# Kernel optimization log

Hardware: AMD Instinct MI355X
Metric: run time of the kernel (lower is better)

The kernel has to match this reference:

```python
import jax, jax.numpy as jnp
import numpy as np

B, N, C = 64, 197, 768
H, GH, D = 12, 2, 64           # num_heads, global_heads, head_dim
HR = H // GH                    # head_ratio = 6
TOTAL_HEADS = 2 * GH + H        # 16
SCALE = D ** -0.5
LEVELS = 3


def setup_inputs() -> dict:
    key = jax.random.key(0)
    ks = jax.random.split(key, 10)
    s = 0.02
    return {
        "x": jax.random.normal(ks[0], (B, N, C), jnp.float32),
        "qkv_w": jax.random.normal(ks[1], (C, TOTAL_HEADS * D), jnp.float32) * s,
        "qkv_b": jax.random.normal(ks[2], (TOTAL_HEADS * D,), jnp.float32) * s,
        "masks": jax.random.uniform(ks[3], (N, N, LEVELS), jnp.float32),
        "mask_proj": jnp.ones((LEVELS, H), jnp.float32),
        "mask_base": jax.random.normal(ks[4], (H,), jnp.float32) * s,
        "head_proj_w": jnp.eye(H, dtype=jnp.float32) + jax.random.normal(ks[5], (H, H), jnp.float32) * s,
        "head_proj_b": jax.random.normal(ks[6], (H,), jnp.float32) * s,
        "proj_w": jax.random.normal(ks[7], (C, C), jnp.float32) * s,
        "proj_b": jax.random.normal(ks[8], (C,), jnp.float32) * s,
    }


def reference(x, qkv_w, qkv_b, masks, mask_proj, mask_base, head_proj_w, head_proj_b, proj_w, proj_b):
    b, n, c = x.shape
    # fused qkv projection -> (b, total_heads, n, d)
    qkv = (x @ qkv_w + qkv_b).reshape(b, n, TOTAL_HEADS, D).transpose(0, 2, 1, 3)
    q = qkv[:, :GH]                 # (b, gh, n, d)
    k = qkv[:, GH:2 * GH]           # (b, gh, n, d)
    v = qkv[:, 2 * GH:]             # (b, h, n, d)

    # global-head attention scores (b, gh, n, n)
    attn = jnp.einsum("bgnd,bgmd->bgnm", q, k) * SCALE

    # per-pair learned mask weights: (n, n, levels) @ (levels, h) -> (n, n, h)
    mw = masks @ mask_proj + mask_base
    # reshape to (1, gh, n, n, hr) per global_proj_type='full'
    mw = mw.reshape(n, n, GH, HR).transpose(2, 0, 1, 3)[None]

    # modulate scores: (b, gh, n, n, hr)
    a = attn[..., None] * mw

    # non_linear head mixing: relu then per-position linear over heads
    a = a.transpose(0, 2, 3, 1, 4).reshape(b, n, n, H)   # (b, n, n, h)
    a = jax.nn.relu(a) @ head_proj_w + head_proj_b
    a = a.transpose(0, 3, 1, 2)                          # (b, h, n, n)

    a = jax.nn.softmax(a, axis=-1)
    out = jnp.einsum("bhnm,bhmd->bnhd", a, v).reshape(b, n, c)
    return out @ proj_w + proj_b
```

## Files before the change

### kernel.cpp

```cpp
#include <hip/hip_runtime.h>
#include <cstdint>
#include <cstddef>

#define BB   64
#define NN   197
#define CC   768
#define HH   12
#define THD  16
#define DD   64
#define MROWS (BB*NN)
#define QKVN (THD*DD)
#define SCALE_ 0.125f
#define ATTS 208
#define KPAD 224
#define SSTR 240

typedef unsigned short u16;
typedef __attribute__((ext_vector_type(2))) float f32x2;
typedef __attribute__((ext_vector_type(4))) float f32x4;
typedef __attribute__((ext_vector_type(8))) short s16x8;
typedef __attribute__((address_space(1))) unsigned int as1_u32;
typedef __attribute__((address_space(3))) unsigned int as3_u32;

__device__ __forceinline__ float bf2f(u16 u) {
  union { unsigned int i; float f; } x; x.i = ((unsigned int)u) << 16; return x.f;
}
__device__ __forceinline__ u16 f2bf(float f) {
  unsigned int x = __builtin_bit_cast(unsigned int, f);
  unsigned int r = (x + 0x7fffu + ((x >> 16) & 1u)) >> 16;
  return (u16)r;
}
__device__ __forceinline__ void gl_lds16(const u16* g, u16* l) {
  __builtin_amdgcn_global_load_lds((const as1_u32*)g, (as3_u32*)l, 16, 0, 0);
}

__global__ __launch_bounds__(256) void k_cvt_x(const float* __restrict__ src,
                                               u16* __restrict__ dst, int n8) {
  int i = blockIdx.x * 256 + threadIdx.x;
  if (i >= n8) return;
  const float4* s = (const float4*)src;
  float4 a = s[2 * i], b = s[2 * i + 1];
  ushort4 lo, hi;
  lo.x = f2bf(a.x); lo.y = f2bf(a.y); lo.z = f2bf(a.z); lo.w = f2bf(a.w);
  hi.x = f2bf(b.x); hi.y = f2bf(b.y); hi.z = f2bf(b.z); hi.w = f2bf(b.w);
  ((ushort4*)dst)[2 * i] = lo;
  ((ushort4*)dst)[2 * i + 1] = hi;
}

__global__ __launch_bounds__(256) void k_transpose(const float* __restrict__ in,
                                                   u16* __restrict__ out,
                                                   int R, int Ccol) {
  __shared__ u16 tile[32][33];
  int c0 = blockIdx.x * 32, r0 = blockIdx.y * 32;
  int tx = threadIdx.x & 31, ty = threadIdx.x >> 5;
#pragma unroll
  for (int i = 0; i < 32; i += 8) {
    int r = r0 + ty + i, c = c0 + tx;
    tile[ty + i][tx] = (r < R && c < Ccol) ? f2bf(in[(size_t)r * Ccol + c]) : (u16)0;
  }
  __syncthreads();
#pragma unroll
  for (int i = 0; i < 32; i += 8) {
    int cc = c0 + ty + i, rr = r0 + tx;
    if (cc < Ccol && rr < R) out[(size_t)cc * R + rr] = tile[tx][ty + i];
  }
}

__global__ __launch_bounds__(512, 2) void k_gemm_bt(const u16* __restrict__ A,
                                                    const u16* __restrict__ Bt,
                                                    const float* __restrict__ bias,
                                                    void* __restrict__ Cout,
                                                    int M, int Nn, int K,
                                                    int write_bf16) {
  __shared__ u16 As[2][2][256 * 32];
  __shared__ u16 Bs[2][2][256 * 32];
  int t = threadIdx.x;
  int w = t >> 6, lane = t & 63;

  int NT = gridDim.y;
  int nwg = gridDim.x * gridDim.y;
  int d = blockIdx.y * gridDim.x + blockIdx.x;
  int q8 = nwg >> 3, r8 = nwg & 7;
  int xcd = d & 7, j = d >> 3;
  int g = (xcd < r8 ? xcd * (q8 + 1) : r8 * (q8 + 1) + (xcd - r8) * q8) + j;
  int mt = g / NT, nt = g - mt * NT;
  int m0 = mt * 256, n0 = nt * 256;

  int wm = w >> 2, wn = w & 3;

  f32x4 acc[8][4];
#pragma unroll
  for (int i = 0; i < 8; i++)
#pragma unroll
    for (int j2 = 0; j2 < 4; j2++)
#pragma unroll
      for (int e = 0; e < 4; e++) acc[i][j2][e] = 0.f;

  int lrow4 = lane >> 2;
  int lkc = (lane & 3) * 8;

  auto stage = [&](int buf, int kbase) {
#pragma unroll
    for (int kh = 0; kh < 2; kh++) {
      int kk = kbase + kh * 32;
#pragma unroll
      for (int rc = 0; rc < 2; rc++) {
        int c = w + rc * 8;
        int row = c * 16 + lrow4;
        int ga = m0 + row; if (ga >= M) ga = M - 1;
        gl_lds16(A + (size_t)ga * K + kk + lkc, &As[buf][kh][c * 512]);
        gl_lds16(Bt + (size_t)(n0 + row) * K + kk + lkc, &Bs[buf][kh][c * 512]);
      }
    }
  };

  auto compute = [&](int buf) {
    int r16 = lane & 15, k8 = (lane >> 4) * 8;
#pragma unroll
    for (int kh = 0; kh < 2; kh++) {
      s16x8 af[8], bfv[4];
#pragma unroll
      for (int s = 0; s < 8; s++)
        af[s]  = *(const s16x8*)&As[buf][kh][(wm * 128 + s * 16 + r16) * 32 + k8];
#pragma unroll
      for (int s = 0; s < 4; s++)
        bfv[s] = *(const s16x8*)&Bs[buf][kh][(wn * 64 + s * 16 + r16) * 32 + k8];
#pragma unroll
      for (int sm = 0; sm < 8; sm++)
#pragma unroll
        for (int sn = 0; sn < 4; sn++)
          acc[sm][sn] = __builtin_amdgcn_mfma_f32_16x16x32_bf16(af[sm], bfv[sn], acc[sm][sn], 0, 0, 0);
    }
  };

  stage(0, 0);
  __syncthreads();
  int cur = 0;
  for (int k0 = 0; k0 < K; k0 += 64) {
    if (k0 + 64 < K) stage(cur ^ 1, k0 + 64);
    compute(cur);
    __syncthreads();
    cur ^= 1;
  }

  u16*   Cb = (u16*)Cout;
  float* Cf = (float*)Cout;
  int quad = lane >> 4, col = lane & 15;
#pragma unroll
  for (int sn = 0; sn < 4; sn++) {
    int gn = n0 + wn * 64 + sn * 16 + col;
    float bv = bias[gn];
#pragma unroll
    for (int sm = 0; sm < 8; sm++) {
      int gmb = m0 + wm * 128 + sm * 16 + quad * 4;
#pragma unroll
      for (int i = 0; i < 4; i++) {
        int gm = gmb + i;
        if (gm < M) {
          float v = acc[sm][sn][i] + bv;
          if (write_bf16) Cb[(size_t)gm * Nn + gn] = f2bf(v);
          else            Cf[(size_t)gm * Nn + gn] = v;
        }
      }
    }
  }
}

__global__ __launch_bounds__(256) void k_qk(const u16* __restrict__ qkv,
                                            float* __restrict__ att) {
  __shared__ u16 As[2][128 * 32];
  __shared__ u16 Bs[2][128 * 32];
  int t = threadIdx.x;
  int w = t >> 6, lane = t & 63;
  int bz = blockIdx.z, b = bz >> 1, g = bz & 1;
  int n0 = blockIdx.x * 128;
  int m0 = blockIdx.y * 128;
  int wm = w >> 1, wn = w & 1;

  f32x4 acc[4][4];
#pragma unroll
  for (int i = 0; i < 4; i++)
#pragma unroll
    for (int j = 0; j < 4; j++)
#pragma unroll
      for (int e = 0; e < 4; e++) acc[i][j][e] = 0.f;

  int lrow4 = lane >> 2, lkc = (lane & 3) * 8;

#pragma unroll
  for (int half = 0; half < 2; half++) {
    int kk = half * 32;
#pragma unroll
    for (int rc = 0; rc < 2; rc++) {
      int c = w + rc * 4;
      int row = c * 16 + lrow4;
      int nq = n0 + row; if (nq > NN - 1) nq = NN - 1;
      int mk = m0 + row; if (mk > NN - 1) mk = NN - 1;
      gl_lds16(qkv + (size_t)(b * NN + nq) * QKVN + g * DD + kk + lkc, &As[half][c * 512]);
      gl_lds16(qkv + (size_t)(b * NN + mk) * QKVN + 2 * DD + g * DD + kk + lkc, &Bs[half][c * 512]);
    }
  }
  __syncthreads();
  {
    int r16 = lane & 15, k8 = (lane >> 4) * 8;
#pragma unroll
    for (int half = 0; half < 2; half++) {
      s16x8 af[4], bfv[4];
#pragma unroll
      for (int s = 0; s < 4; s++) {
        af[s]  = *(const s16x8*)&As[half][(wm * 64 + s * 16 + r16) * 32 + k8];
        bfv[s] = *(const s16x8*)&Bs[half][(wn * 64 + s * 16 + r16) * 32 + k8];
      }
#pragma unroll
      for (int sm = 0; sm < 4; sm++)
#pragma unroll
        for (int sn = 0; sn < 4; sn++)
          acc[sm][sn] = __builtin_amdgcn_mfma_f32_16x16x32_bf16(af[sm], bfv[sn], acc[sm][sn], 0, 0, 0);
    }
  }
  int quad = lane >> 4, col = lane & 15;
#pragma unroll
  for (int sn = 0; sn < 4; sn++) {
    int gn = m0 + wn * 64 + sn * 16 + col;
#pragma unroll
    for (int sm = 0; sm < 4; sm++) {
      int gmb = n0 + wm * 64 + sm * 16 + quad * 4;
#pragma unroll
      for (int i = 0; i < 4; i++) {
        int gm = gmb + i;
        if (gm < NN && gn < NN)
          att[((size_t)bz * NN + gm) * ATTS + gn] = acc[sm][sn][i] * SCALE_;
      }
    }
  }
}

__global__ __launch_bounds__(256) void k_softmax_p(const float* __restrict__ att,
                                                   const float* __restrict__ masks,
                                                   const float* __restrict__ mproj,
                                                   const float* __restrict__ mbase,
                                                   const float* __restrict__ hpw,
                                                   const float* __restrict__ hpb,
                                                   u16* __restrict__ P) {
  __shared__ float S[12][SSTR];
  __shared__ f32x2 hpw_s[72];
  __shared__ f32x2 mp_s[18];
  __shared__ f32x2 mb_s[6], hpb_s[6];
  __shared__ float inv_s[12];
  int t = threadIdx.x;
  int n = blockIdx.x, b = blockIdx.y;

  if (t < 72) hpw_s[t] = ((const f32x2*)hpw)[t];
  if (t < 18) mp_s[t] = ((const f32x2*)mproj)[t];
  if (t < 6) { mb_s[t] = ((const f32x2*)mbase)[t]; hpb_s[t] = ((const f32x2*)hpb)[t]; }
  __syncthreads();

  if (t < NN) {
    int m = t;
    float a0 = att[((size_t)(b * 2 + 0) * NN + n) * ATTS + m];
    float a1 = att[((size_t)(b * 2 + 1) * NN + n) * ATTS + m];
    const float* mk = masks + ((size_t)n * NN + m) * 3;
    float l0 = mk[0], l1 = mk[1], l2 = mk[2];
    f32x2 pre2[6];
#pragma unroll
    for (int k = 0; k < 6; k++) {
      f32x2 wv = mb_s[k] + l0 * mp_s[k] + l1 * mp_s[6 + k] + l2 * mp_s[12 + k];
      float av = (k < 3) ? a0 : a1;
      f32x2 v = wv * av;
      pre2[k].x = v.x > 0.f ? v.x : 0.f;
      pre2[k].y = v.y > 0.f ? v.y : 0.f;
    }
    f32x2 s2[6];
#pragma unroll
    for (int k = 0; k < 6; k++) s2[k] = hpb_s[k];
#pragma unroll
    for (int h = 0; h < 12; h++) {
      float p = (h & 1) ? pre2[h >> 1].y : pre2[h >> 1].x;
#pragma unroll
      for (int k = 0; k < 6; k++) s2[k] += p * hpw_s[h * 6 + k];
    }
#pragma unroll
    for (int k = 0; k < 6; k++) {
      S[2 * k][m] = s2[k].x;
      S[2 * k + 1][m] = s2[k].y;
    }
  } else if (t < KPAD) {
#pragma unroll
    for (int h = 0; h < 12; h++) S[h][t] = 0.f;
  }
  __syncthreads();

  {
    int g = t >> 4, l16 = t & 15;
    if (g < 12) {
      float vals[13];
      float mx = -1e30f;
#pragma unroll
      for (int i = 0; i < 13; i++) {
        int m = l16 + i * 16;
        float x = S[g][m];
        vals[i] = (m < NN) ? x : -1e30f;
        mx = fmaxf(mx, vals[i]);
      }
#pragma unroll
      for (int off = 8; off; off >>= 1) mx = fmaxf(mx, __shfl_xor(mx, off, 16));
      float sum = 0.f;
#pragma unroll
      for (int i = 0; i < 13; i++) {
        int m = l16 + i * 16;
        float e = __expf(vals[i] - mx);
        if (m < NN) { S[g][m] = e; sum += e; }
      }
#pragma unroll
      for (int off = 8; off; off >>= 1) sum += __shfl_xor(sum, off, 16);
      if (l16 == 0) inv_s[g] = 1.f / sum;
    }
  }
  __syncthreads();

  for (int c4 = t; c4 < 672; c4 += 256) {
    int h = c4 / 56;
    int m = (c4 - h * 56) * 4;
    f32x4 v = *(const f32x4*)&S[h][m];
    float iv = inv_s[h];
    ushort4 u;
    u.x = f2bf(v.x * iv); u.y = f2bf(v.y * iv);
    u.z = f2bf(v.z * iv); u.w = f2bf(v.w * iv);
    *(ushort4*)(P + ((size_t)(b * HH + h) * NN + n) * KPAD + m) = u;
  }
}

__global__ __launch_bounds__(256) void k_pv(const u16* __restrict__ P,
                                            const u16* __restrict__ qkv,
                                            u16* __restrict__ aout) {
  __shared__ u16 As[2][128 * 32];
  __shared__ u16 Bs[2][64 * 32];
  int t = threadIdx.x;
  int w = t >> 6, lane = t & 63;
  int bh = blockIdx.y, b = bh / HH, h = bh - b * HH;
  int n0 = blockIdx.x * 128;

  f32x4 acc[2][4];
#pragma unroll
  for (int i = 0; i < 2; i++)
#pragma unroll
    for (int j = 0; j < 4; j++)
#pragma unroll
      for (int e = 0; e < 4; e++) acc[i][j][e] = 0.f;

  int lrow4 = lane >> 2, lkc = (lane & 3) * 8;
  int vml = t & 31, vd0 = (t >> 5) * 8;

  for (int k0 = 0; k0 < KPAD; k0 += 64) {
    int nh = (KPAD - k0 >= 64) ? 2 : 1;
    for (int half = 0; half < nh; half++) {
      int kk = k0 + half * 32;
#pragma unroll
      for (int rc = 0; rc < 2; rc++) {
        int c = w + rc * 4;
        int row = c * 16 + lrow4;
        int gn = n0 + row; if (gn > NN - 1) gn = NN - 1;
        gl_lds16(P + ((size_t)bh * NN + gn) * KPAD + kk + lkc, &As[half][c * 512]);
      }
      {
        int m = kk + vml;
        u16 v8[8];
        if (m < NN) {
          const ushort4* vp = (const ushort4*)(qkv + (size_t)(b * NN + m) * QKVN + (4 + h) * DD + vd0);
          ushort4 lo = vp[0], hi = vp[1];
          v8[0] = lo.x; v8[1] = lo.y; v8[2] = lo.z; v8[3] = lo.w;
          v8[4] = hi.x; v8[5] = hi.y; v8[6] = hi.z; v8[7] = hi.w;
        } else {
#pragma unroll
          for (int j = 0; j < 8; j++) v8[j] = 0;
        }
#pragma unroll
        for (int j = 0; j < 8; j++) Bs[half][(vd0 + j) * 32 + vml] = v8[j];
      }
    }
    __syncthreads();
    int r16 = lane & 15, k8 = (lane >> 4) * 8;
    for (int half = 0; half < nh; half++) {
      s16x8 af[2], bfv[4];
#pragma unroll
      for (int s = 0; s < 2; s++)
        af[s] = *(const s16x8*)&As[half][(w * 32 + s * 16 + r16) * 32 + k8];
#pragma unroll
      for (int s = 0; s < 4; s++)
        bfv[s] = *(const s16x8*)&Bs[half][(s * 16 + r16) * 32 + k8];
#pragma unroll
      for (int sm = 0; sm < 2; sm++)
#pragma unroll
        for (int sn = 0; sn < 4; sn++)
          acc[sm][sn] = __builtin_amdgcn_mfma_f32_16x16x32_bf16(af[sm], bfv[sn], acc[sm][sn], 0, 0, 0);
    }
    __syncthreads();
  }
  int quad = lane >> 4, col = lane & 15;
#pragma unroll
  for (int sn = 0; sn < 4; sn++) {
    int gd = sn * 16 + col;
#pragma unroll
    for (int sm = 0; sm < 2; sm++) {
      int gnb = n0 + w * 32 + sm * 16 + quad * 4;
#pragma unroll
      for (int i = 0; i < 4; i++) {
        int gn = gnb + i;
        if (gn < NN)
          aout[(size_t)(b * NN + gn) * CC + h * DD + gd] = f2bf(acc[sm][sn][i]);
      }
    }
  }
}

extern "C" void kernel_launch(void* const* d_in, const int* in_sizes, int n_in,
                              void* d_out, int out_size, void* d_ws, size_t ws_size,
                              hipStream_t stream) {
  const float* x     = (const float*)d_in[0];
  const float* qkv_w = (const float*)d_in[1];
  const float* qkv_b = (const float*)d_in[2];
  const float* masks = (const float*)d_in[3];
  const float* mproj = (const float*)d_in[4];
  const float* mbase = (const float*)d_in[5];
  const float* hpw   = (const float*)d_in[6];
  const float* hpb   = (const float*)d_in[7];
  const float* projw = (const float*)d_in[8];
  const float* projb = (const float*)d_in[9];

  char* ws = (char*)d_ws;
  size_t off = 0;
  auto alloc = [&](size_t bytes) {
    char* p = ws + off; off = (off + bytes + 255) & ~(size_t)255; return p;
  };
  char*  r1   = alloc((size_t)BB * 2 * NN * ATTS * 4);
  u16*   xbf  = (u16*)r1;
  float* att  = (float*)r1;
  u16*   aout = (u16*)r1;
  u16*   qkv  = (u16*)alloc((size_t)MROWS * QKVN * 2);
  u16*   P    = (u16*)alloc((size_t)BB * HH * NN * KPAD * 2);
  u16*   wt1  = (u16*)alloc((size_t)QKVN * CC * 2);
  u16*   wt2  = (u16*)alloc((size_t)CC * CC * 2);

  int n8 = MROWS * CC / 8;
  k_cvt_x<<<(n8 + 255) / 256, 256, 0, stream>>>(x, xbf, n8);
  k_transpose<<<dim3(QKVN / 32, CC / 32), 256, 0, stream>>>(qkv_w, wt1, CC, QKVN);
  k_transpose<<<dim3(CC / 32, CC / 32), 256, 0, stream>>>(projw, wt2, CC, CC);
  k_gemm_bt<<<dim3((MROWS + 255) / 256, QKVN / 256), 512, 0, stream>>>(
      xbf, wt1, qkv_b, qkv, MROWS, QKVN, CC, 1);
  k_qk<<<dim3(2, 2, BB * 2), 256, 0, stream>>>(qkv, att);
  k_softmax_p<<<dim3(NN, BB), 256, 0, stream>>>(att, masks, mproj, mbase, hpw, hpb, P);
  k_pv<<<dim3(2, BB * HH), 256, 0, stream>>>(P, qkv, aout);
  k_gemm_bt<<<dim3((MROWS + 255) / 256, CC / 256), 512, 0, stream>>>(
      aout, wt2, projb, d_out, MROWS, CC, CC, 0);
}
```

Measured before the change: 275.7 us.

## Triple-buffer GEMM LDS stages with K=32 steps and explicit vmcnt waits

The bf16 GEMM kernel moves from a double-buffered K=64 staging loop to a three-stage ring of K=32 LDS buffers. It keeps two tiles in flight and waits on vmcnt counts instead of full syncthreads. The aim is to hide global-to-LDS load latency behind MFMA compute while using less LDS per block. The trade-off is more barriers per K and reliance on exact vmcnt accounting for correctness.

```diff
diff --git a/kernel.cpp b/kernel.cpp
--- a/kernel.cpp
+++ b/kernel.cpp
@@ -72,8 +72,8 @@
                                                     void* __restrict__ Cout,
                                                     int M, int Nn, int K,
                                                     int write_bf16) {
-  __shared__ u16 As[2][2][256 * 32];
-  __shared__ u16 Bs[2][2][256 * 32];
+  __shared__ u16 As[3][256 * 32];
+  __shared__ u16 Bs[3][256 * 32];
   int t = threadIdx.x;
   int w = t >> 6, lane = t & 63;
 
@@ -83,8 +83,8 @@
   int q8 = nwg >> 3, r8 = nwg & 7;
   int xcd = d & 7, j = d >> 3;
   int g = (xcd < r8 ? xcd * (q8 + 1) : r8 * (q8 + 1) + (xcd - r8) * q8) + j;
-  int mt = g / NT, nt = g - mt * NT;
-  int m0 = mt * 256, n0 = nt * 256;
+  int mt = g / NT, nt_ = g - mt * NT;
+  int m0 = mt * 256, n0 = nt_ * 256;
 
   int wm = w >> 2, wn = w & 3;
 
@@ -99,49 +99,53 @@
   int lrow4 = lane >> 2;
   int lkc = (lane & 3) * 8;
 
-  auto stage = [&](int buf, int kbase) {
-#pragma unroll
-    for (int kh = 0; kh < 2; kh++) {
-      int kk = kbase + kh * 32;
-#pragma unroll
-      for (int rc = 0; rc < 2; rc++) {
-        int c = w + rc * 8;
-        int row = c * 16 + lrow4;
-        int ga = m0 + row; if (ga >= M) ga = M - 1;
-        gl_lds16(A + (size_t)ga * K + kk + lkc, &As[buf][kh][c * 512]);
-        gl_lds16(Bt + (size_t)(n0 + row) * K + kk + lkc, &Bs[buf][kh][c * 512]);
-      }
+  auto stage = [&](int buf, int kk) {
+#pragma unroll
+    for (int rc = 0; rc < 2; rc++) {
+      int c = w + rc * 8;
+      int row = c * 16 + lrow4;
+      int ga = m0 + row; if (ga >= M) ga = M - 1;
+      gl_lds16(A + (size_t)ga * K + kk + lkc, &As[buf][c * 512]);
+      gl_lds16(Bt + (size_t)(n0 + row) * K + kk + lkc, &Bs[buf][c * 512]);
     }
   };
 
   auto compute = [&](int buf) {
     int r16 = lane & 15, k8 = (lane >> 4) * 8;
-#pragma unroll
-    for (int kh = 0; kh < 2; kh++) {
-      s16x8 af[8], bfv[4];
-#pragma unroll
-      for (int s = 0; s < 8; s++)
-        af[s]  = *(const s16x8*)&As[buf][kh][(wm * 128 + s * 16 + r16) * 32 + k8];
-#pragma unroll
-      for (int s = 0; s < 4; s++)
-        bfv[s] = *(const s16x8*)&Bs[buf][kh][(wn * 64 + s * 16 + r16) * 32 + k8];
-#pragma unroll
-      for (int sm = 0; sm < 8; sm++)
-#pragma unroll
-        for (int sn = 0; sn < 4; sn++)
-          acc[sm][sn] = __builtin_amdgcn_mfma_f32_16x16x32_bf16(af[sm], bfv[sn], acc[sm][sn], 0, 0, 0);
-    }
+    s16x8 af[8], bfv[4];
+#pragma unroll
+    for (int s = 0; s < 8; s++)
+      af[s] = *(const s16x8*)&As[buf][(wm * 128 + s * 16 + r16) * 32 + k8];
+#pragma unroll
+    for (int s = 0; s < 4; s++)
+      bfv[s] = *(const s16x8*)&Bs[buf][(wn * 64 + s * 16 + r16) * 32 + k8];
+#pragma unroll
+    for (int sm = 0; sm < 8; sm++)
+#pragma unroll
+      for (int sn = 0; sn < 4; sn++)
+        acc[sm][sn] = __builtin_amdgcn_mfma_f32_16x16x32_bf16(af[sm], bfv[sn], acc[sm][sn], 0, 0, 0);
   };
 
+  int nt = K >> 5;
   stage(0, 0);
-  __syncthreads();
-  int cur = 0;
-  for (int k0 = 0; k0 < K; k0 += 64) {
-    if (k0 + 64 < K) stage(cur ^ 1, k0 + 64);
-    compute(cur);
-    __syncthreads();
-    cur ^= 1;
-  }
+  stage(1, 32);
+  for (int tt = 0; tt < nt - 2; ++tt) {
+    stage((tt + 2) % 3, (tt + 2) * 32);
+    asm volatile("s_waitcnt vmcnt(8)" ::: "memory");
+    __builtin_amdgcn_sched_barrier(0);
+    __builtin_amdgcn_s_barrier();
+    compute(tt % 3);
+    __builtin_amdgcn_s_barrier();
+  }
+  asm volatile("s_waitcnt vmcnt(4)" ::: "memory");
+  __builtin_amdgcn_sched_barrier(0);
+  __builtin_amdgcn_s_barrier();
+  compute((nt - 2) % 3);
+  __builtin_amdgcn_s_barrier();
+  asm volatile("s_waitcnt vmcnt(0)" ::: "memory");
+  __builtin_amdgcn_sched_barrier(0);
+  __builtin_amdgcn_s_barrier();
+  compute((nt - 1) % 3);
 
   u16*   Cb = (u16*)Cout;
   float* Cf = (float*)Cout;
```

Measured after the change: 274.3 us. No clear change (-0.5%).
